# Optimization experiments

Measured on AMD Instinct MI355X. Metric: run time of the kernel, lower is better.

## Reference

```python
import jax, jax.numpy as jnp
import numpy as np

N, E, D, L, G = 50000, 800000, 128, 3, 64
DIM_OUT = 10
EPS_BN = 1e-5
EPS_AGG = 1e-6


def setup_inputs() -> dict:
    key = jax.random.key(0)
    ks = jax.random.split(key, 10)
    x = jax.random.normal(ks[0], (N, D), jnp.float32)
    edge_attr = jax.random.normal(ks[1], (E, D), jnp.float32)
    edge_index = jax.random.randint(ks[2], (2, E), 0, N)
    batch_vec = jnp.sort(jax.random.randint(ks[3], (N,), 0, G))
    s = 1.0 / np.sqrt(D)
    def w(k, shape):
        return jax.random.uniform(k, shape, jnp.float32, -s, s)
    lin_w = w(ks[4], (L, 4, D, D))   # per-layer stacked A,B,D,E weights
    lin_b = w(ks[5], (L, 4, D))
    bn_gamma = jnp.ones((L, D), jnp.float32)
    bn_beta = jnp.zeros((L, D), jnp.float32)
    post_w1 = w(ks[6], (D, D)); post_b1 = w(ks[7], (D,))
    post_w2 = w(ks[8], (D, DIM_OUT)); post_b2 = w(ks[9], (DIM_OUT,))
    return dict(x=x, edge_attr=edge_attr, edge_index=edge_index, batch_vec=batch_vec,
                lin_w=lin_w, lin_b=lin_b, bn_gamma=bn_gamma, bn_beta=bn_beta,
                post_w1=post_w1, post_b1=post_b1, post_w2=post_w2, post_b2=post_b2)


def _batchnorm_train(h, gamma, beta):
    # training-mode BN over node dim (biased variance, as in torch)
    mu = h.mean(0)
    var = h.var(0)
    return (h - mu) * jax.lax.rsqrt(var + EPS_BN) * gamma + beta


def reference(x, edge_attr, edge_index, batch_vec, lin_w, lin_b, bn_gamma, bn_beta,
              post_w1, post_b1, post_w2, post_b2):
    src, dst = edge_index[0], edge_index[1]   # j -> i (source_to_target)
    e = edge_attr
    for l in range(L):
        x_in = x
        # fused A,B,D,E projections: [4, N, D]
        proj = jnp.einsum('nd,kdo->kno', x, lin_w[l]) + lin_b[l][:, None, :]
        Ax, Bx, Dx, Ex = proj[0], proj[1], proj[2], proj[3]
        e_ij = Dx[dst] + Ex[src]                # [E, D]
        sigma = jax.nn.sigmoid(e_ij)
        num = jax.ops.segment_sum(sigma * Bx[src], dst, num_segments=N)
        den = jax.ops.segment_sum(sigma, dst, num_segments=N)
        h = Ax + num / (den + EPS_AGG)
        h = jax.nn.relu(_batchnorm_train(h, bn_gamma[l], bn_beta[l]))
        x = x_in + h                            # residual
        e = e_ij                                # edge features updated (bn_edge_e unused in forward)
    counts = jax.ops.segment_sum(jnp.ones((N,), x.dtype), batch_vec, num_segments=G)
    pooled = jax.ops.segment_sum(x, batch_vec, num_segments=G) / jnp.maximum(counts, 1.0)[:, None]
    h = jax.nn.relu(pooled @ post_w1 + post_b1)
    return h @ post_w2 + post_b2                # [G, DIM_OUT]
```

## Files before the change

### kernel.cpp

```cpp
#include <hip/hip_runtime.h>
#include <math.h>

constexpr int N_NODES = 50000;
constexpr int N_EDGES = 800000;
constexpr int DIM     = 128;
constexpr int NLAYERS = 3;
constexpr int NGRAPH  = 64;
constexpr int DOUT    = 10;
constexpr float EPS_BN  = 1e-5f;
constexpr float EPS_AGG = 1e-6f;

typedef __attribute__((ext_vector_type(8))) short   bf16x8;
typedef __attribute__((ext_vector_type(4))) float   floatx4;
typedef __attribute__((ext_vector_type(4))) unsigned short ushort4v;

__device__ inline unsigned short f2bf(float f) {
    union { float f; unsigned int u; } v; v.f = f;
    unsigned int u = v.u;
    return (unsigned short)((u + 0x7fffu + ((u >> 16) & 1u)) >> 16);
}

__global__ void hist_kernel(const int* __restrict__ dst, int* __restrict__ cnt) {
    int e = blockIdx.x * 256 + threadIdx.x;
    if (e < N_EDGES) atomicAdd(&cnt[dst[e]], 1);
}

__global__ void scan1_kernel(const int* __restrict__ cnt, int* __restrict__ row_ptr,
                             int* __restrict__ partials) {
    __shared__ int s[256];
    int i = blockIdx.x * 256 + threadIdx.x;
    int v = (i < N_NODES) ? cnt[i] : 0;
    s[threadIdx.x] = v;
    __syncthreads();
    for (int off = 1; off < 256; off <<= 1) {
        int t = (threadIdx.x >= off) ? s[threadIdx.x - off] : 0;
        __syncthreads();
        s[threadIdx.x] += t;
        __syncthreads();
    }
    if (i < N_NODES) row_ptr[i] = s[threadIdx.x] - v;
    if (threadIdx.x == 255) partials[blockIdx.x] = s[255];
}

__global__ void scan2_kernel(int* partials, int nb) {
    __shared__ int s[256];
    int t = threadIdx.x;
    int v = (t < nb) ? partials[t] : 0;
    s[t] = v;
    __syncthreads();
    for (int off = 1; off < 256; off <<= 1) {
        int u = (t >= off) ? s[t - off] : 0;
        __syncthreads();
        s[t] += u;
        __syncthreads();
    }
    if (t < nb) partials[t] = s[t] - v;
}

__global__ void scan3_kernel(int* row_ptr, const int* __restrict__ partials) {
    int i = blockIdx.x * 256 + threadIdx.x;
    if (i < N_NODES) row_ptr[i] += partials[blockIdx.x];
    if (blockIdx.x == 0 && threadIdx.x == 0) row_ptr[N_NODES] = N_EDGES;
}

__global__ void scatter_kernel(const int* __restrict__ src, const int* __restrict__ dst,
                               const int* __restrict__ row_ptr, int* __restrict__ cursor,
                               int* __restrict__ col_src) {
    int e = blockIdx.x * 256 + threadIdx.x;
    if (e < N_EDGES) {
        int d = dst[e];
        int pos = row_ptr[d] + atomicAdd(&cursor[d], 1);
        col_src[pos] = src[e];
    }
}

__global__ void wconv_kernel(const float* __restrict__ W, unsigned short* __restrict__ Wt) {
    int idx = blockIdx.x * 256 + threadIdx.x;
    int c = idx & 127, d = (idx >> 7) & 127, lk = idx >> 14;
    Wt[((size_t)lk * 128 + c) * 128 + d] = f2bf(W[idx]);
}

__global__ __launch_bounds__(256) void xinit_kernel(const float* __restrict__ x_in,
                                                    float* __restrict__ x_cur,
                                                    unsigned short* __restrict__ xb) {
    int i4 = blockIdx.x * 256 + threadIdx.x;
    float4 v = *(const float4*)&x_in[(size_t)i4 * 4];
    *(float4*)&x_cur[(size_t)i4 * 4] = v;
    ushort4v b; b.x = f2bf(v.x); b.y = f2bf(v.y); b.z = f2bf(v.z); b.w = f2bf(v.w);
    *(ushort4v*)&xb[(size_t)i4 * 4] = b;
}

__global__ __launch_bounds__(256) void gemm_mfma(const unsigned short* __restrict__ xb,
                                                 const unsigned short* __restrict__ Wt,
                                                 const float* __restrict__ bias,
                                                 float* __restrict__ proj) {
    const int ksl = blockIdx.y;
    const int m0  = blockIdx.x * 128;
    const int tid = threadIdx.x;
    const int wave = tid >> 6, lane = tid & 63;
    const int wm = (wave >> 1) * 64, wc = (wave & 1) * 64;
    const int quad = lane >> 4, l16 = lane & 15;
    const unsigned short* Wk = Wt + (size_t)ksl * DIM * DIM;

    floatx4 acc[4][4];
#pragma unroll
    for (int i = 0; i < 4; i++)
#pragma unroll
        for (int j = 0; j < 4; j++) acc[i][j] = (floatx4)0.f;

#pragma unroll
    for (int ks = 0; ks < 4; ks++) {
        const int kk = ks * 32 + quad * 8;
        bf16x8 a[4], b[4];
#pragma unroll
        for (int i = 0; i < 4; i++) {
            int row = m0 + wm + i * 16 + l16;
            row = min(row, N_NODES - 1);
            a[i] = *(const bf16x8*)&xb[(size_t)row * DIM + kk];
        }
#pragma unroll
        for (int j = 0; j < 4; j++) {
            int col = wc + j * 16 + l16;
            b[j] = *(const bf16x8*)&Wk[(size_t)col * DIM + kk];
        }
#pragma unroll
        for (int i = 0; i < 4; i++)
#pragma unroll
            for (int j = 0; j < 4; j++)
                acc[i][j] = __builtin_amdgcn_mfma_f32_16x16x32_bf16(a[i], b[j], acc[i][j], 0, 0, 0);
    }

    float bv[4];
#pragma unroll
    for (int j = 0; j < 4; j++) bv[j] = bias[ksl * DIM + wc + j * 16 + l16];

#pragma unroll
    for (int i = 0; i < 4; i++) {
#pragma unroll
        for (int r = 0; r < 4; r++) {
            int row = m0 + wm + i * 16 + quad * 4 + r;
            if (row >= N_NODES) continue;
            float* op = proj + ((size_t)ksl * N_NODES + row) * DIM;
#pragma unroll
            for (int j = 0; j < 4; j++)
                op[wc + j * 16 + l16] = acc[i][j][r] + bv[j];
        }
    }
}

__global__ __launch_bounds__(128) void agg_kernel(float* proj,
                                                  const int* __restrict__ row_ptr,
                                                  const int* __restrict__ col_src) {
    const int i = blockIdx.x;
    const int d = threadIdx.x;
    const float* Bx = proj + (size_t)1 * N_NODES * DIM;
    const float* Dx = proj + (size_t)2 * N_NODES * DIM;
    const float* Ex = proj + (size_t)3 * N_NODES * DIM;

    const float dx = Dx[(size_t)i * DIM + d];
    float num = 0.f, den = 0.f;
    const int e0 = row_ptr[i], e1 = row_ptr[i + 1];
    int e = e0;
    for (; e + 1 < e1; e += 2) {
        int s0 = col_src[e], s1 = col_src[e + 1];
        float ex0 = Ex[(size_t)s0 * DIM + d];
        float bx0 = Bx[(size_t)s0 * DIM + d];
        float ex1 = Ex[(size_t)s1 * DIM + d];
        float bx1 = Bx[(size_t)s1 * DIM + d];
        float sg0 = 1.f / (1.f + __expf(-(dx + ex0)));
        float sg1 = 1.f / (1.f + __expf(-(dx + ex1)));
        num += sg0 * bx0 + sg1 * bx1;
        den += sg0 + sg1;
    }
    if (e < e1) {
        int s = col_src[e];
        float ex = Ex[(size_t)s * DIM + d];
        float bx = Bx[(size_t)s * DIM + d];
        float sg = 1.f / (1.f + __expf(-(dx + ex)));
        num += sg * bx;
        den += sg;
    }
    float ax = proj[(size_t)i * DIM + d];
    proj[(size_t)i * DIM + d] = ax + num / (den + EPS_AGG);
}

__global__ __launch_bounds__(256) void bnstat_kernel(const float* __restrict__ h,
                                                     float* __restrict__ bn_sum,
                                                     float* __restrict__ bn_sumsq) {
    __shared__ float ss[256], sq[256];
    int t = threadIdx.x;
    int d = t & 127, half = t >> 7;
    int r0 = blockIdx.x * 256;
    float s = 0.f, q = 0.f;
    for (int r = r0 + half; r < r0 + 256 && r < N_NODES; r += 2) {
        float v = h[(size_t)r * DIM + d];
        s += v; q += v * v;
    }
    ss[t] = s; sq[t] = q;
    __syncthreads();
    if (t < 128) {
        atomicAdd(&bn_sum[d], ss[t] + ss[t + 128]);
        atomicAdd(&bn_sumsq[d], sq[t] + sq[t + 128]);
    }
}

__global__ void bnfin_kernel(const float* __restrict__ bn_sum, const float* __restrict__ bn_sumsq,
                             const float* __restrict__ gamma, const float* __restrict__ beta,
                             float* __restrict__ scale, float* __restrict__ shift) {
    int d = threadIdx.x;
    float mu  = bn_sum[d] * (1.f / N_NODES);
    float var = bn_sumsq[d] * (1.f / N_NODES) - mu * mu;
    float sc  = gamma[d] * rsqrtf(var + EPS_BN);
    scale[d] = sc;
    shift[d] = beta[d] - mu * sc;
}

__global__ __launch_bounds__(256) void apply_kernel(const float* __restrict__ h,
                                                    const float* __restrict__ scale,
                                                    const float* __restrict__ shift,
                                                    float* __restrict__ x,
                                                    unsigned short* __restrict__ xb) {
    int i4 = blockIdx.x * 256 + threadIdx.x;
    int d  = (i4 * 4) & 127;
    float4 hv = *(const float4*)&h[(size_t)i4 * 4];
    float4 xv = *(float4*)&x[(size_t)i4 * 4];
    xv.x += fmaxf(hv.x * scale[d + 0] + shift[d + 0], 0.f);
    xv.y += fmaxf(hv.y * scale[d + 1] + shift[d + 1], 0.f);
    xv.z += fmaxf(hv.z * scale[d + 2] + shift[d + 2], 0.f);
    xv.w += fmaxf(hv.w * scale[d + 3] + shift[d + 3], 0.f);
    *(float4*)&x[(size_t)i4 * 4] = xv;
    ushort4v b; b.x = f2bf(xv.x); b.y = f2bf(xv.y); b.z = f2bf(xv.z); b.w = f2bf(xv.w);
    *(ushort4v*)&xb[(size_t)i4 * 4] = b;
}

__global__ __launch_bounds__(128) void pool_kernel(const float* __restrict__ x,
                                                   const int* __restrict__ batch,
                                                   float* __restrict__ pooled,
                                                   int* __restrict__ gcount) {
    int d = threadIdx.x;
    int r0 = blockIdx.x * 256;
    int r1 = min(r0 + 256, N_NODES);
    int curg = batch[r0];
    float acc = 0.f;
    int run = 0;
    for (int r = r0; r < r1; r++) {
        int g = batch[r];
        if (g != curg) {
            atomicAdd(&pooled[curg * DIM + d], acc);
            if (d == 0) atomicAdd(&gcount[curg], run);
            acc = 0.f; run = 0; curg = g;
        }
        acc += x[(size_t)r * DIM + d];
        run++;
    }
    atomicAdd(&pooled[curg * DIM + d], acc);
    if (d == 0) atomicAdd(&gcount[curg], run);
}

__global__ __launch_bounds__(128) void head_kernel(const float* __restrict__ pooled,
                                                   const int* __restrict__ gcount,
                                                   const float* __restrict__ w1,
                                                   const float* __restrict__ b1,
                                                   const float* __restrict__ w2,
                                                   const float* __restrict__ b2,
                                                   float* __restrict__ out) {
    __shared__ float sp[128], sh[128];
    int g = blockIdx.x, d = threadIdx.x;
    float c = (float)max(gcount[g], 1);
    sp[d] = pooled[g * DIM + d] / c;
    __syncthreads();
    float acc = b1[d];
    for (int dd = 0; dd < DIM; dd++) acc += sp[dd] * w1[dd * DIM + d];
    sh[d] = fmaxf(acc, 0.f);
    __syncthreads();
    if (d < DOUT) {
        float o = b2[d];
        for (int dd = 0; dd < DIM; dd++) o += sh[dd] * w2[dd * DOUT + d];
        out[g * DOUT + d] = o;
    }
}

extern "C" void kernel_launch(void* const* d_in, const int* in_sizes, int n_in,
                              void* d_out, int out_size, void* d_ws, size_t ws_size,
                              hipStream_t stream) {
    const float* x_in  = (const float*)d_in[0];
    const int*   eidx  = (const int*)d_in[2];
    const int*   batch = (const int*)d_in[3];
    const float* lin_w = (const float*)d_in[4];
    const float* lin_b = (const float*)d_in[5];
    const float* gamma = (const float*)d_in[6];
    const float* beta  = (const float*)d_in[7];
    const float* w1    = (const float*)d_in[8];
    const float* b1    = (const float*)d_in[9];
    const float* w2    = (const float*)d_in[10];
    const float* b2    = (const float*)d_in[11];
    float* out = (float*)d_out;

    const int* src = eidx;
    const int* dst = eidx + N_EDGES;

    auto al = [](size_t v) { return (v + 255) & ~(size_t)255; };
    size_t off = 0;
    size_t o_xcur = off; off = al(off + (size_t)N_NODES * DIM * 4);
    size_t o_xb   = off; off = al(off + (size_t)N_NODES * DIM * 2);
    size_t o_wt   = off; off = al(off + (size_t)NLAYERS * 4 * DIM * DIM * 2);
    size_t o_proj = off; off = al(off + (size_t)4 * N_NODES * DIM * 4);
    size_t o_rp   = off; off = al(off + (size_t)(N_NODES + 1) * 4);
    size_t o_cs   = off; off = al(off + (size_t)N_EDGES * 4);
    size_t o_cnt  = off; off = al(off + (size_t)N_NODES * 4);
    size_t o_part = off; off = al(off + 256 * 4);
    size_t o_bn   = off; off = al(off + 512 * 4);
    size_t o_pool = off; off = al(off + (size_t)NGRAPH * DIM * 4);
    size_t o_gc   = off; off = al(off + (size_t)NGRAPH * 4);
    size_t total  = off;

    char* base = (ws_size >= total) ? (char*)d_ws : (char*)d_in[1];

    float*          x_cur    = (float*)(base + o_xcur);
    unsigned short* xb       = (unsigned short*)(base + o_xb);
    unsigned short* Wt       = (unsigned short*)(base + o_wt);
    float*          proj     = (float*)(base + o_proj);
    int*            row_ptr  = (int*)  (base + o_rp);
    int*            col_src  = (int*)  (base + o_cs);
    int*            cnt      = (int*)  (base + o_cnt);
    int*            partials = (int*)  (base + o_part);
    float*          bn_sum   = (float*)(base + o_bn);
    float*          bn_sumsq = bn_sum + 128;
    float*          bn_scale = bn_sum + 256;
    float*          bn_shift = bn_sum + 384;
    float*          pooled   = (float*)(base + o_pool);
    int*            gcount   = (int*)  (base + o_gc);

    const int nbN = (N_NODES + 255) / 256;
    const int nbE = (N_EDGES + 255) / 256;
    const int nb4 = (N_NODES * DIM / 4) / 256;

    xinit_kernel<<<nb4, 256, 0, stream>>>(x_in, x_cur, xb);
    wconv_kernel<<<(NLAYERS * 4 * DIM * DIM) / 256, 256, 0, stream>>>(lin_w, Wt);

    hipMemsetAsync(cnt, 0, (size_t)N_NODES * 4, stream);
    hist_kernel<<<nbE, 256, 0, stream>>>(dst, cnt);
    scan1_kernel<<<nbN, 256, 0, stream>>>(cnt, row_ptr, partials);
    scan2_kernel<<<1, 256, 0, stream>>>(partials, nbN);
    scan3_kernel<<<nbN, 256, 0, stream>>>(row_ptr, partials);
    hipMemsetAsync(cnt, 0, (size_t)N_NODES * 4, stream);
    scatter_kernel<<<nbE, 256, 0, stream>>>(src, dst, row_ptr, cnt, col_src);

    for (int l = 0; l < NLAYERS; l++) {
        gemm_mfma<<<dim3((N_NODES + 127) / 128, 4), 256, 0, stream>>>(
            xb, Wt + (size_t)l * 4 * DIM * DIM, lin_b + (size_t)l * 4 * DIM, proj);
        agg_kernel<<<N_NODES, 128, 0, stream>>>(proj, row_ptr, col_src);
        hipMemsetAsync(bn_sum, 0, 256 * 4, stream);
        bnstat_kernel<<<nbN, 256, 0, stream>>>(proj, bn_sum, bn_sumsq);
        bnfin_kernel<<<1, 128, 0, stream>>>(bn_sum, bn_sumsq, gamma + l * DIM, beta + l * DIM,
                                            bn_scale, bn_shift);
        apply_kernel<<<nb4, 256, 0, stream>>>(proj, bn_scale, bn_shift, x_cur, xb);
    }

    hipMemsetAsync(pooled, 0, (size_t)NGRAPH * DIM * 4, stream);
    hipMemsetAsync(gcount, 0, (size_t)NGRAPH * 4, stream);
    pool_kernel<<<nbN, 128, 0, stream>>>(x_cur, batch, pooled, gcount);
    head_kernel<<<NGRAPH, 128, 0, stream>>>(pooled, gcount, w1, b1, w2, b2, out);
}
```

Baseline: 1.249 ms.

## Pack Bx and Ex as interleaved bf16 pairs for edge gather

The GEMM epilogue now writes the Bx and Ex projections as bf16, interleaved into one 32-bit word per node and feature, while Ax and Dx stay fp32 in separate buffers. The aggregation kernel then fetches both source values with a single 4-byte load per edge instead of two fp32 loads, which halves the gathered bytes on the memory-bound edge loop. Its inner loop is also unrolled from 2 to 4 edges to keep more loads in flight. The cost is reduced precision for the edge terms, and the GEMM epilogue does strided 2-byte stores into the interleaved buffer.

```diff
diff --git a/kernel.cpp b/kernel.cpp
--- a/kernel.cpp
+++ b/kernel.cpp
@@ -19,6 +19,10 @@
     unsigned int u = v.u;
     return (unsigned short)((u + 0x7fffu + ((u >> 16) & 1u)) >> 16);
 }
+__device__ inline float bf2f(unsigned short h) {
+    union { unsigned int u; float f; } v; v.u = ((unsigned int)h) << 16;
+    return v.f;
+}
 
 __global__ void hist_kernel(const int* __restrict__ dst, int* __restrict__ cnt) {
     int e = blockIdx.x * 256 + threadIdx.x;
@@ -93,7 +97,9 @@
 __global__ __launch_bounds__(256) void gemm_mfma(const unsigned short* __restrict__ xb,
                                                  const unsigned short* __restrict__ Wt,
                                                  const float* __restrict__ bias,
-                                                 float* __restrict__ proj) {
+                                                 float* __restrict__ Axh,
+                                                 float* __restrict__ Dx,
+                                                 unsigned int* __restrict__ EB) {
     const int ksl = blockIdx.y;
     const int m0  = blockIdx.x * 128;
     const int tid = threadIdx.x;
@@ -134,54 +140,69 @@
 #pragma unroll
     for (int j = 0; j < 4; j++) bv[j] = bias[ksl * DIM + wc + j * 16 + l16];
 
+    float* fdst = (ksl == 0) ? Axh : Dx;
+    unsigned short* ebp = (unsigned short*)EB;
+    const int half = (ksl == 3) ? 1 : 0;
+
 #pragma unroll
     for (int i = 0; i < 4; i++) {
 #pragma unroll
         for (int r = 0; r < 4; r++) {
             int row = m0 + wm + i * 16 + quad * 4 + r;
             if (row >= N_NODES) continue;
-            float* op = proj + ((size_t)ksl * N_NODES + row) * DIM;
-#pragma unroll
-            for (int j = 0; j < 4; j++)
-                op[wc + j * 16 + l16] = acc[i][j][r] + bv[j];
+            if ((ksl & 1) == 0) {
+                float* op = fdst + (size_t)row * DIM;
+#pragma unroll
+                for (int j = 0; j < 4; j++)
+                    op[wc + j * 16 + l16] = acc[i][j][r] + bv[j];
+            } else {
+                unsigned short* op = ebp + (size_t)row * DIM * 2 + half;
+#pragma unroll
+                for (int j = 0; j < 4; j++)
+                    op[(wc + j * 16 + l16) * 2] = f2bf(acc[i][j][r] + bv[j]);
+            }
         }
     }
 }
 
-__global__ __launch_bounds__(128) void agg_kernel(float* proj,
+__global__ __launch_bounds__(128) void agg_kernel(float* __restrict__ Axh,
+                                                  const float* __restrict__ Dx,
+                                                  const unsigned int* __restrict__ EB,
                                                   const int* __restrict__ row_ptr,
                                                   const int* __restrict__ col_src) {
     const int i = blockIdx.x;
     const int d = threadIdx.x;
-    const float* Bx = proj + (size_t)1 * N_NODES * DIM;
-    const float* Dx = proj + (size_t)2 * N_NODES * DIM;
-    const float* Ex = proj + (size_t)3 * N_NODES * DIM;
 
     const float dx = Dx[(size_t)i * DIM + d];
     float num = 0.f, den = 0.f;
     const int e0 = row_ptr[i], e1 = row_ptr[i + 1];
     int e = e0;
-    for (; e + 1 < e1; e += 2) {
+    for (; e + 3 < e1; e += 4) {
         int s0 = col_src[e], s1 = col_src[e + 1];
-        float ex0 = Ex[(size_t)s0 * DIM + d];
-        float bx0 = Bx[(size_t)s0 * DIM + d];
-        float ex1 = Ex[(size_t)s1 * DIM + d];
-        float bx1 = Bx[(size_t)s1 * DIM + d];
-        float sg0 = 1.f / (1.f + __expf(-(dx + ex0)));
-        float sg1 = 1.f / (1.f + __expf(-(dx + ex1)));
-        num += sg0 * bx0 + sg1 * bx1;
-        den += sg0 + sg1;
-    }
-    if (e < e1) {
+        int s2 = col_src[e + 2], s3 = col_src[e + 3];
+        unsigned int w0 = EB[(size_t)s0 * DIM + d];
+        unsigned int w1 = EB[(size_t)s1 * DIM + d];
+        unsigned int w2 = EB[(size_t)s2 * DIM + d];
+        unsigned int w3 = EB[(size_t)s3 * DIM + d];
+        float sg0 = 1.f / (1.f + __expf(-(dx + bf2f((unsigned short)(w0 >> 16)))));
+        float sg1 = 1.f / (1.f + __expf(-(dx + bf2f((unsigned short)(w1 >> 16)))));
+        float sg2 = 1.f / (1.f + __expf(-(dx + bf2f((unsigned short)(w2 >> 16)))));
+        float sg3 = 1.f / (1.f + __expf(-(dx + bf2f((unsigned short)(w3 >> 16)))));
+        num += sg0 * bf2f((unsigned short)(w0 & 0xffff))
+             + sg1 * bf2f((unsigned short)(w1 & 0xffff))
+             + sg2 * bf2f((unsigned short)(w2 & 0xffff))
+             + sg3 * bf2f((unsigned short)(w3 & 0xffff));
+        den += sg0 + sg1 + sg2 + sg3;
+    }
+    for (; e < e1; e++) {
         int s = col_src[e];
-        float ex = Ex[(size_t)s * DIM + d];
-        float bx = Bx[(size_t)s * DIM + d];
-        float sg = 1.f / (1.f + __expf(-(dx + ex)));
-        num += sg * bx;
+        unsigned int w = EB[(size_t)s * DIM + d];
+        float sg = 1.f / (1.f + __expf(-(dx + bf2f((unsigned short)(w >> 16)))));
+        num += sg * bf2f((unsigned short)(w & 0xffff));
         den += sg;
     }
-    float ax = proj[(size_t)i * DIM + d];
-    proj[(size_t)i * DIM + d] = ax + num / (den + EPS_AGG);
+    float ax = Axh[(size_t)i * DIM + d];
+    Axh[(size_t)i * DIM + d] = ax + num / (den + EPS_AGG);
 }
 
 __global__ __launch_bounds__(256) void bnstat_kernel(const float* __restrict__ h,
@@ -304,7 +325,9 @@
     size_t o_xcur = off; off = al(off + (size_t)N_NODES * DIM * 4);
     size_t o_xb   = off; off = al(off + (size_t)N_NODES * DIM * 2);
     size_t o_wt   = off; off = al(off + (size_t)NLAYERS * 4 * DIM * DIM * 2);
-    size_t o_proj = off; off = al(off + (size_t)4 * N_NODES * DIM * 4);
+    size_t o_axh  = off; off = al(off + (size_t)N_NODES * DIM * 4);
+    size_t o_dx   = off; off = al(off + (size_t)N_NODES * DIM * 4);
+    size_t o_eb   = off; off = al(off + (size_t)N_NODES * DIM * 4);
     size_t o_rp   = off; off = al(off + (size_t)(N_NODES + 1) * 4);
     size_t o_cs   = off; off = al(off + (size_t)N_EDGES * 4);
     size_t o_cnt  = off; off = al(off + (size_t)N_NODES * 4);
@@ -319,7 +342,9 @@
     float*          x_cur    = (float*)(base + o_xcur);
     unsigned short* xb       = (unsigned short*)(base + o_xb);
     unsigned short* Wt       = (unsigned short*)(base + o_wt);
-    float*          proj     = (float*)(base + o_proj);
+    float*          Axh      = (float*)(base + o_axh);
+    float*          Dx       = (float*)(base + o_dx);
+    unsigned int*   EB       = (unsigned int*)(base + o_eb);
     int*            row_ptr  = (int*)  (base + o_rp);
     int*            col_src  = (int*)  (base + o_cs);
     int*            cnt      = (int*)  (base + o_cnt);
@@ -348,13 +373,13 @@
 
     for (int l = 0; l < NLAYERS; l++) {
         gemm_mfma<<<dim3((N_NODES + 127) / 128, 4), 256, 0, stream>>>(
-            xb, Wt + (size_t)l * 4 * DIM * DIM, lin_b + (size_t)l * 4 * DIM, proj);
-        agg_kernel<<<N_NODES, 128, 0, stream>>>(proj, row_ptr, col_src);
+            xb, Wt + (size_t)l * 4 * DIM * DIM, lin_b + (size_t)l * 4 * DIM, Axh, Dx, EB);
+        agg_kernel<<<N_NODES, 128, 0, stream>>>(Axh, Dx, EB, row_ptr, col_src);
         hipMemsetAsync(bn_sum, 0, 256 * 4, stream);
-        bnstat_kernel<<<nbN, 256, 0, stream>>>(proj, bn_sum, bn_sumsq);
+        bnstat_kernel<<<nbN, 256, 0, stream>>>(Axh, bn_sum, bn_sumsq);
         bnfin_kernel<<<1, 128, 0, stream>>>(bn_sum, bn_sumsq, gamma + l * DIM, beta + l * DIM,
                                             bn_scale, bn_shift);
-        apply_kernel<<<nb4, 256, 0, stream>>>(proj, bn_scale, bn_shift, x_cur, xb);
+        apply_kernel<<<nb4, 256, 0, stream>>>(Axh, bn_scale, bn_shift, x_cur, xb);
     }
 
     hipMemsetAsync(pooled, 0, (size_t)NGRAPH * DIM * 4, stream);
```

New measurement: 1.128 ms. -9.7%, faster.
